# Kernel tuning notes

Hardware: AMD Instinct MI355X
Metric: run time of the kernel (lower is better)

Reference implementation:

```python
import jax, jax.numpy as jnp
import numpy as np

NMS_THR = 0.7
TOPK = 128      # fixed post-NMS rois per level (static padding for jit)
OUT = 14        # RoIAlign output size
SAMPLES = 2     # samples per bin per dim (fixed approximation of sampling_ratio=-1)
STRIDES = (32.0, 16.0, 8.0)


def get_channel(a):
    # a: [..., 4] boxes as (cx, cy, w, h); FPN level assignment, clamped to [1, 4]
    s = jnp.sqrt(a[..., 2] * a[..., 3])
    return jnp.clip(jnp.floor(3.0 + jnp.log2(s / 224.0)), 1.0, 4.0)


def cxcywh_to_xyxy(b):
    cx, cy, w, h = b[..., 0], b[..., 1], b[..., 2], b[..., 3]
    return jnp.stack([cx - w / 2, cy - h / 2, cx + w / 2, cy + h / 2], axis=-1)


def pairwise_iou(b):
    x1, y1, x2, y2 = b[:, 0], b[:, 1], b[:, 2], b[:, 3]
    area = jnp.maximum(x2 - x1, 0.0) * jnp.maximum(y2 - y1, 0.0)
    ix1 = jnp.maximum(x1[:, None], x1[None, :])
    iy1 = jnp.maximum(y1[:, None], y1[None, :])
    ix2 = jnp.minimum(x2[:, None], x2[None, :])
    iy2 = jnp.minimum(y2[:, None], y2[None, :])
    inter = jnp.maximum(ix2 - ix1, 0.0) * jnp.maximum(iy2 - iy1, 0.0)
    union = area[:, None] + area[None, :] - inter
    return inter / jnp.maximum(union, 1e-9)


def nms_keep(boxes_xyxy, scores, thr):
    # Greedy NMS over masked scores (-inf entries sort last and are excluded later).
    n = scores.shape[0]
    order = jnp.argsort(-scores)
    iou = pairwise_iou(boxes_xyxy[order])  # [N, N]
    idx = jnp.arange(n)

    def body(sup, i):
        keep_i = ~sup[i]
        sup = sup | (keep_i & (iou[i] > thr) & (idx > i))
        return sup, keep_i

    _, keeps_sorted = jax.lax.scan(body, jnp.zeros(n, dtype=bool), idx)
    return jnp.zeros(n, dtype=bool).at[order].set(keeps_sorted)


def roi_align(feat, boxes):
    # feat: [C, H, W]; boxes: [K, 4]. NOTE: the original prepare_boxes feeds
    # (cx, cy, w, h) straight into RoIAlign, which interprets them as
    # (x1, y1, x2, y2) -- replicated faithfully here. spatial_scale = 1.
    C, H, W = feat.shape
    K = boxes.shape[0]
    x1, y1, x2, y2 = boxes[:, 0], boxes[:, 1], boxes[:, 2], boxes[:, 3]
    rw = jnp.maximum(x2 - x1, 1.0)
    rh = jnp.maximum(y2 - y1, 1.0)
    bw = rw / OUT
    bh = rh / OUT
    # fractional bin offsets, [OUT*SAMPLES]
    f = (jnp.arange(OUT, dtype=feat.dtype)[:, None]
         + (jnp.arange(SAMPLES, dtype=feat.dtype)[None, :] + 0.5) / SAMPLES).reshape(-1)
    ys = y1[:, None] + bh[:, None] * f[None, :]  # [K, S]
    xs = x1[:, None] + bw[:, None] * f[None, :]
    Y = ys[:, :, None]  # [K, S, 1]
    X = xs[:, None, :]  # [K, 1, S]
    valid = (Y > -1.0) & (Y < H) & (X > -1.0) & (X < W)  # [K, S, S]
    Yc = jnp.clip(Y, 0.0, H - 1.0)
    Xc = jnp.clip(X, 0.0, W - 1.0)
    y0 = jnp.floor(Yc)
    x0 = jnp.floor(Xc)
    y0i = y0.astype(jnp.int32)
    x0i = x0.astype(jnp.int32)
    y1i = jnp.minimum(y0i + 1, H - 1)
    x1i = jnp.minimum(x0i + 1, W - 1)
    ly = Yc - y0
    lx = Xc - x0
    hy = 1.0 - ly
    hx = 1.0 - lx
    g = lambda yi, xi: feat[:, yi, xi]  # -> [C, K, S, S]
    val = (g(y0i, x0i) * (hy * hx) + g(y0i, x1i) * (hy * lx)
           + g(y1i, x0i) * (ly * hx) + g(y1i, x1i) * (ly * lx))
    val = val * valid.astype(val.dtype)
    val = val.reshape(C, K, OUT, SAMPLES, OUT, SAMPLES).mean(axis=(3, 5))
    return jnp.transpose(val, (1, 0, 2, 3))  # [K, C, OUT, OUT]


def level_extract(feat, boxes, scores, levs, nl):
    # one image, one target FPN level: mask, NMS, fixed top-K select, RoIAlign
    mask = levs == nl
    msc = jnp.where(mask, scores, -jnp.inf)
    xyxy = cxcywh_to_xyxy(boxes)
    keep = nms_keep(jax.lax.stop_gradient(xyxy), jax.lax.stop_gradient(msc), NMS_THR)
    eff = jnp.where(keep & mask, msc, -jnp.inf)
    vals, sel = jax.lax.top_k(jax.lax.stop_gradient(eff), TOPK)
    valid = jnp.isfinite(vals)
    rois = boxes[sel] * valid[:, None].astype(boxes.dtype)
    out = roi_align(feat, rois)
    return out * valid[:, None, None, None].astype(out.dtype)


def _forward(p32, p16, p8, p4, a32, a16, a8, s32, s16, s8):
    anchors = (a32, a16, a8)  # p4 proposals are computed then discarded in the
    # original (grouping loop only runs l in range(3)); p4 features are never
    # RoIAligned either (nl loops 1..3), so p4 only appears as an unused input.
    levs = jnp.concatenate([get_channel(a) for a in anchors], axis=1)      # [B, N]
    boxes = jnp.concatenate([a * s for a, s in zip(anchors, STRIDES)], axis=1)
    scores = jnp.concatenate([s32, s16, s8], axis=1)
    outs = []
    for nl, feat in zip((1.0, 2.0, 3.0), (p32, p16, p8)):
        fn = jax.vmap(lambda f, b, s, l, nl=nl: level_extract(f, b, s, l, nl))
        outs.append(fn(feat, boxes, scores, levs))  # [B, TOPK, C, 14, 14]
    return jnp.concatenate(outs, axis=1)  # [B, 3*TOPK, C, 14, 14]


def setup_inputs():
    key = jax.random.key(0)
    ks = jax.random.split(key, 10)
    B, C = 2, 256
    p32 = jax.random.normal(ks[0], (B, C, 32, 32), jnp.float32)
    p16 = jax.random.normal(ks[1], (B, C, 64, 64), jnp.float32)
    p8 = jax.random.normal(ks[2], (B, C, 128, 128), jnp.float32)
    p4 = jax.random.normal(ks[3], (B, C, 256, 256), jnp.float32)

    def mk_anchors(k, n, hf):
        k1, k2 = jax.random.split(k)
        cxy = jax.random.uniform(k1, (B, n, 2), jnp.float32) * hf
        wh = 16.0 + jax.random.uniform(k2, (B, n, 2), jnp.float32) * 434.0
        return jnp.concatenate([cxy, wh], axis=-1)

    anchors_32 = mk_anchors(ks[4], 512, 32.0)
    anchors_16 = mk_anchors(ks[5], 1024, 64.0)
    anchors_8 = mk_anchors(ks[6], 2048, 128.0)
    scores_32 = jax.random.normal(ks[7], (B, 512), jnp.float32)
    scores_16 = jax.random.normal(ks[8], (B, 1024), jnp.float32)
    scores_8 = jax.random.normal(ks[9], (B, 2048), jnp.float32)
    return dict(p32=p32, p16=p16, p8=p8, p4=p4,
                anchors_32=anchors_32, anchors_16=anchors_16, anchors_8=anchors_8,
                scores_32=scores_32, scores_16=scores_16, scores_8=scores_8)


def reference(p32, p16, p8, p4, anchors_32, anchors_16, anchors_8,
              scores_32, scores_16, scores_8):
    return _forward(p32, p16, p8, p4, anchors_32, anchors_16, anchors_8,
                    scores_32, scores_16, scores_8)
```

## Files before the change

### kernel.cpp

```cpp
#include <hip/hip_runtime.h>
#include <stdint.h>

#define NMS_THR 0.7f
#define TOPK 128
#define NTOT 3584
#define CAP 2048
#define OUTSZ 14
#define NSAMP 28
#define OUT_VF4 (768 * 12544)

typedef unsigned long long u64;
typedef float vf4 __attribute__((ext_vector_type(4)));
typedef float float2u __attribute__((ext_vector_type(2), aligned(4)));

__device__ __forceinline__ u64 shfl_xor64(u64 v, int mask) {
    int lo = __shfl_xor((int)(unsigned)v, mask);
    int hi = __shfl_xor((int)(v >> 32), mask);
    return ((u64)(unsigned)hi << 32) | (unsigned)lo;
}
__device__ __forceinline__ u64 shfl64(u64 v, int src) {
    int lo = __shfl((int)(unsigned)v, src);
    int hi = __shfl((int)(v >> 32), src);
    return ((u64)(unsigned)hi << 32) | (unsigned)lo;
}
__device__ __forceinline__ void cex_shfl(u64 &e, int t, int j, int k) {
    u64 p = shfl_xor64(e, j);
    bool up = ((t & k) == 0);
    bool lower = ((t & j) == 0);
    u64 mn = (e < p) ? e : p;
    u64 mx = (e < p) ? p : e;
    e = (lower == up) ? mn : mx;
}
__device__ __forceinline__ float boxarea(float4 b) {
    return __fmul_rn(fmaxf(__fsub_rn(b.z, b.x), 0.0f),
                     fmaxf(__fsub_rn(b.w, b.y), 0.0f));
}

__device__ __forceinline__ void fetch_anchor(
    const float* __restrict__ a32, const float* __restrict__ a16,
    const float* __restrict__ a8,
    const float* __restrict__ s32, const float* __restrict__ s16,
    const float* __restrict__ s8,
    int b, int i, float* A, float* st, float* sc)
{
    const float* P;
    if (i < 512) {
        P = a32 + (b * 512 + i) * 4;  *st = 32.0f; *sc = s32[b * 512 + i];
    } else if (i < 1536) {
        int j = i - 512;
        P = a16 + (b * 1024 + j) * 4; *st = 16.0f; *sc = s16[b * 1024 + j];
    } else {
        int j = i - 1536;
        P = a8 + (b * 2048 + j) * 4;  *st = 8.0f;  *sc = s8[b * 2048 + j];
    }
    float4 v = *(const float4*)P;
    A[0] = v.x; A[1] = v.y; A[2] = v.z; A[3] = v.w;
}

__global__ __launch_bounds__(1024) void select_kernel(
    const float* __restrict__ a32, const float* __restrict__ a16,
    const float* __restrict__ a8,
    const float* __restrict__ s32, const float* __restrict__ s16,
    const float* __restrict__ s8,
    float* __restrict__ rois,
    int* __restrict__ validOut,
    float* __restrict__ out)
{
    int tid = threadIdx.x;

    if (blockIdx.x >= 6) {
        vf4 z = (vf4)0.0f;
        vf4* O4 = (vf4*)out;
        int stride = (gridDim.x - 6) * 1024;
        for (int i = (blockIdx.x - 6) * 1024 + tid; i < OUT_VF4; i += stride)
            O4[i] = z;
        return;
    }

    __shared__ u64 keysup[CAP];
    __shared__ float4 cbox4[CAP];
    __shared__ int sidx[CAP];
    __shared__ float4 kb4[TOPK];
    __shared__ float karea[TOPK];
    __shared__ u64 extw[16];
    __shared__ int selList[TOPK];
    __shared__ int mCount, keptSh;

    int prob = blockIdx.x;
    int b = prob / 3;
    int nl = prob % 3 + 1;
    int lane = tid & 63;
    int wv = tid >> 6;
    int t0 = (wv << 7) + lane;
    int t1 = t0 + 64;

    if (tid == 0) mCount = 0;
    __syncthreads();

    for (int i = tid; i < NTOT; i += 1024) {
        float A[4], st, sc;
        fetch_anchor(a32, a16, a8, s32, s16, s8, b, i, A, &st, &sc);
        float s = sqrtf(__fmul_rn(A[2], A[3]));
        float lv = floorf(__fadd_rn(3.0f, log2f(__fdiv_rn(s, 224.0f))));
        lv = fminf(fmaxf(lv, 1.0f), 4.0f);
        if ((int)lv == nl) {
            unsigned u = __float_as_uint(sc);
            u = (u & 0x80000000u) ? ~u : (u | 0x80000000u);
            unsigned d = ~u;
            int pos = atomicAdd(&mCount, 1);
            if (pos < CAP) keysup[pos] = ((u64)d << 32) | (unsigned)i;
        }
    }
    __syncthreads();
    int m = mCount;
    if (m > CAP) m = CAP;
    for (int i = m + tid; i < CAP; i += 1024) keysup[i] = ~0ull;
    __syncthreads();

    {
        u64 e0 = keysup[t0], e1 = keysup[t1];
        for (int k = 2; k <= 128; k <<= 1) {
            int jstart = k >> 1;
            if (k == 128) {
                bool up = ((t0 & k) == 0);
                if ((e0 > e1) == up) { u64 tmp = e0; e0 = e1; e1 = tmp; }
                jstart = 32;
            }
            for (int j = jstart; j > 0; j >>= 1) {
                cex_shfl(e0, t0, j, k);
                cex_shfl(e1, t1, j, k);
            }
        }
        keysup[t0] = e0; keysup[t1] = e1;
    }
    __syncthreads();
    for (int k = 256; k <= 2048; k <<= 1) {
        for (int j = k >> 1; j >= 128; j >>= 1) {
            for (int t = tid; t < CAP; t += 1024) {
                int ixj = t ^ j;
                if (ixj > t) {
                    u64 a = keysup[t], bb = keysup[ixj];
                    bool up = ((t & k) == 0);
                    if ((a > bb) == up) { keysup[t] = bb; keysup[ixj] = a; }
                }
            }
            __syncthreads();
        }
        {
            u64 e0 = keysup[t0], e1 = keysup[t1];
            bool up = ((t0 & k) == 0);
            if ((e0 > e1) == up) { u64 tmp = e0; e0 = e1; e1 = tmp; }
            for (int j = 32; j > 0; j >>= 1) {
                cex_shfl(e0, t0, j, k);
                cex_shfl(e1, t1, j, k);
            }
            keysup[t0] = e0; keysup[t1] = e1;
        }
        __syncthreads();
    }

    for (int r = tid; r < m; r += 1024) {
        int orig = (int)(keysup[r] & 0xffffffffu);
        sidx[r] = orig;
        float A[4], st, sc;
        fetch_anchor(a32, a16, a8, s32, s16, s8, b, orig, A, &st, &sc);
        float cx = A[0] * st, cy = A[1] * st, w = A[2] * st, h = A[3] * st;
        float4 v;
        v.x = __fsub_rn(cx, 0.5f * w);
        v.y = __fsub_rn(cy, 0.5f * h);
        v.z = __fadd_rn(cx, 0.5f * w);
        v.w = __fadd_rn(cy, 0.5f * h);
        cbox4[r] = v;
    }
    __syncthreads();

    int nch = (m + 63) >> 6;
    for (int c = wv; c < nch; c += 16) {
        int base = c << 6;
        int n = m - base; if (n > 64) n = 64;
        float4 cb = cbox4[base + ((lane < n) ? lane : 0)];
        float car = boxarea(cb);
        for (int i = 0; i < n; i++) {
            float4 ib = cbox4[base + i];
            float iar = boxarea(ib);
            float i1 = fmaxf(ib.x, cb.x), i2 = fmaxf(ib.y, cb.y);
            float i3 = fminf(ib.z, cb.z), i4 = fminf(ib.w, cb.w);
            float inr = __fmul_rn(fmaxf(__fsub_rn(i3, i1), 0.0f),
                                  fmaxf(__fsub_rn(i4, i2), 0.0f));
            float unr = __fsub_rn(__fadd_rn(iar, car), inr);
            bool bit = (lane < n) && (lane > i) &&
                       (__fdiv_rn(inr, fmaxf(unr, 1e-9f)) > NMS_THR);
            u64 bal = __ballot(bit);
            if (lane == 0) keysup[base + i] = bal;
        }
    }
    __syncthreads();

    int kept = 0;
    for (int c = 0; c < nch && kept < TOPK; c++) {
        int base = c << 6;
        int n = m - base; if (n > 64) n = 64;

        float4 cb = cbox4[base + ((lane < n) ? lane : 0)];
        float car = boxarea(cb);
        bool s = false;
        for (int kk = wv; kk < kept; kk += 16) {
            float4 kb = kb4[kk]; float kar = karea[kk];
            float i1 = fmaxf(kb.x, cb.x), i2 = fmaxf(kb.y, cb.y);
            float i3 = fminf(kb.z, cb.z), i4 = fminf(kb.w, cb.w);
            float inr = __fmul_rn(fmaxf(__fsub_rn(i3, i1), 0.0f),
                                  fmaxf(__fsub_rn(i4, i2), 0.0f));
            float unr = __fsub_rn(__fadd_rn(kar, car), inr);
            if (__fdiv_rn(inr, fmaxf(unr, 1e-9f)) > NMS_THR) s = true;
        }
        u64 bal = __ballot(s);
        if (lane == 0) extw[wv] = bal;
        __syncthreads();

        if (wv == 0) {
            u64 ext = 0;
            #pragma unroll
            for (int i = 0; i < 16; i++) ext |= extw[i];
            u64 row = keysup[base + lane];
            bool alive = (lane < n) && !((ext >> lane) & 1ull);
            int nk = kept;
            while (nk < TOPK) {
                u64 b2 = __ballot(alive);
                if (b2 == 0ull) break;
                int pick = __builtin_ctzll(b2);
                if (lane == 0) selList[nk] = base + pick;
                if (lane == 1) {
                    float4 pb = cbox4[base + pick];
                    kb4[nk] = pb; karea[nk] = boxarea(pb);
                }
                u64 prow = shfl64(row, pick);
                alive = alive && !((prow >> lane) & 1ull) && (lane != pick);
                nk++;
            }
            if (lane == 0) keptSh = nk;
        }
        __syncthreads();
        kept = keptSh;
    }

    for (int k = tid; k < TOPK; k += 1024) {
        float4 rv = make_float4(0.0f, 0.0f, 0.0f, 0.0f);
        int vld = 0;
        if (k < kept) {
            int orig = sidx[selList[k]];
            float A[4], st, sc;
            fetch_anchor(a32, a16, a8, s32, s16, s8, b, orig, A, &st, &sc);
            rv = make_float4(A[0] * st, A[1] * st, A[2] * st, A[3] * st);
            vld = 1;
        }
        ((float4*)rois)[prob * TOPK + k] = rv;
        validOut[prob * TOPK + k] = vld;
    }
}

__global__ __launch_bounds__(256) void roialign_kernel(
    const float* __restrict__ p32, const float* __restrict__ p16,
    const float* __restrict__ p8,
    const float* __restrict__ rois, const int* __restrict__ validIn,
    float* __restrict__ out)
{
    int roiIdx = blockIdx.x;
    int b = roiIdx / 384;
    int slot = roiIdx - b * 384;
    int lvl = slot / TOPK;
    int k = slot - lvl * TOPK;
    int prob = b * 3 + lvl;
    int tid = threadIdx.x;

    int vld = validIn[prob * TOPK + k];
    if (!vld) return;

    float* O = out + (size_t)roiIdx * 256 * 196;

    int W;
    const float* feat;
    if (lvl == 0)      { W = 32;  feat = p32; }
    else if (lvl == 1) { W = 64;  feat = p16; }
    else               { W = 128; feat = p8; }
    int HW = W * W;
    const float* F0 = feat + (size_t)b * 256 * HW;

    __shared__ int sxb[NSAMP], sy0[NSAMP], sy1[NSAMP];
    __shared__ float swx0[NSAMP], swx1[NSAMP], shy[NSAMP], sly[NSAMP];
    __shared__ int sxv[NSAMP], syv[NSAMP];
    __shared__ int oiL[OUTSZ], ojL[OUTSZ];
    __shared__ int nyx[2];

    if (tid < 2 * NSAMP) {
        const float* R = rois + ((size_t)prob * TOPK + k) * 4;
        float x1 = R[0], y1 = R[1], x2 = R[2], y2 = R[3];
        float rw = fmaxf(__fsub_rn(x2, x1), 1.0f);
        float rh = fmaxf(__fsub_rn(y2, y1), 1.0f);
        float bw = __fdiv_rn(rw, 14.0f);
        float bh = __fdiv_rn(rh, 14.0f);
        int axis = tid / NSAMP;
        int s = tid - axis * NSAMP;
        float fi = (float)(s >> 1) + ((s & 1) ? 0.75f : 0.25f);
        float start = axis ? y1 : x1;
        float bsz = axis ? bh : bw;
        float lim = (float)W;
        float X = __fadd_rn(start, __fmul_rn(bsz, fi));
        bool v = (X > -1.0f) && (X < lim);
        float Xc = fminf(fmaxf(X, 0.0f), lim - 1.0f);
        float x0f = floorf(Xc);
        int x0 = (int)x0f;
        float l = __fsub_rn(Xc, x0f);
        float hh = __fsub_rn(1.0f, l);
        float vf = v ? 1.0f : 0.0f;
        if (axis == 0) {
            int base; float w0, w1;
            if (x0 >= W - 1) { base = W - 2; w0 = 0.0f; w1 = vf; }
            else             { base = x0;    w0 = hh * vf; w1 = l * vf; }
            sxb[s] = base; swx0[s] = w0; swx1[s] = w1; sxv[s] = v ? 1 : 0;
        } else {
            sy0[s] = x0; sy1[s] = min(x0 + 1, W - 1);
            shy[s] = hh * vf; sly[s] = l * vf; syv[s] = v ? 1 : 0;
        }
    }
    __syncthreads();

    if (tid == 0) {
        int n = 0;
        for (int oi = 0; oi < OUTSZ; oi++)
            if (syv[2 * oi] | syv[2 * oi + 1]) oiL[n++] = oi;
        nyx[0] = n;
    }
    if (tid == 1) {
        int n = 0;
        for (int oj = 0; oj < OUTSZ; oj++)
            if (sxv[2 * oj] | sxv[2 * oj + 1]) ojL[n++] = oj;
        nyx[1] = n;
    }
    __syncthreads();

    int ny = nyx[0], nx = nyx[1];
    int total = ny * nx;
    if (total == 0) return;

    int w = tid >> 6;
    int lane = tid & 63;

    for (int ci = w; ci < total; ci += 4) {
        int oi = oiL[ci / nx];
        int oj = ojL[ci - (ci / nx) * nx];
        int sA = oi * 2, sB = sA + 1;
        int tA = oj * 2, tB = tA + 1;
        int y0A = sy0[sA], y1A = sy1[sA], y0B = sy0[sB], y1B = sy1[sB];
        float hyA = shy[sA], lyA = sly[sA], hyB = shy[sB], lyB = sly[sB];
        int xA = sxb[tA], xB = sxb[tB];
        float xw0A = swx0[tA], xw1A = swx1[tA];
        float xw0B = swx0[tB], xw1B = swx1[tB];
        int p = oi * 14 + oj;

        for (int it = 0; it < 4; it++) {
            int c = lane + it * 64;
            const float* F = F0 + c * HW;
            const float* rA0 = F + y0A * W;
            const float* rA1 = F + y1A * W;
            const float* rB0 = F + y0B * W;
            const float* rB1 = F + y1B * W;

            float2u a0 = *(const float2u*)(rA0 + xA);
            float2u a1 = *(const float2u*)(rA1 + xA);
            float2u c0 = *(const float2u*)(rA0 + xB);
            float2u c1 = *(const float2u*)(rA1 + xB);
            float2u b0 = *(const float2u*)(rB0 + xA);
            float2u b1 = *(const float2u*)(rB1 + xA);
            float2u d0 = *(const float2u*)(rB0 + xB);
            float2u d1 = *(const float2u*)(rB1 + xB);

            float s00 = hyA * (xw0A * a0.x + xw1A * a0.y) + lyA * (xw0A * a1.x + xw1A * a1.y);
            float s01 = hyA * (xw0B * c0.x + xw1B * c0.y) + lyA * (xw0B * c1.x + xw1B * c1.y);
            float s10 = hyB * (xw0A * b0.x + xw1A * b0.y) + lyB * (xw0A * b1.x + xw1A * b1.y);
            float s11 = hyB * (xw0B * d0.x + xw1B * d0.y) + lyB * (xw0B * d1.x + xw1B * d1.y);
            O[c * 196 + p] = 0.25f * (s00 + s01 + s10 + s11);
        }
    }
}

extern "C" void kernel_launch(void* const* d_in, const int* in_sizes, int n_in,
                              void* d_out, int out_size, void* d_ws, size_t ws_size,
                              hipStream_t stream) {
    const float* p32 = (const float*)d_in[0];
    const float* p16 = (const float*)d_in[1];
    const float* p8  = (const float*)d_in[2];
    const float* a32 = (const float*)d_in[4];
    const float* a16 = (const float*)d_in[5];
    const float* a8  = (const float*)d_in[6];
    const float* s32 = (const float*)d_in[7];
    const float* s16 = (const float*)d_in[8];
    const float* s8  = (const float*)d_in[9];
    float* out = (float*)d_out;

    const size_t totalFloats = 3072 + 768;

    float* base;
    if (ws_size >= totalFloats * 4) {
        base = (float*)d_ws;
    } else {
        base = (float*)d_in[3];
    }
    float* rois  = base;
    int*   valid = (int*)(base + 3072);

    select_kernel<<<768, 1024, 0, stream>>>(a32, a16, a8, s32, s16, s8,
                                            rois, valid, out);
    roialign_kernel<<<768, 256, 0, stream>>>(p32, p16, p8, rois, valid, out);
}
```

Baseline: 362.1 us.

## Drop precomputed suppression matrix, compute IoU on the fly in 256-box chunks

Removes the all-pairs 64x64 suppression bitmask precompute. The serial greedy NMS now works on 256-candidate chunks: a single wave tracks four alive masks and evaluates each picked box's IoU against its candidates on the fly. The change also compacts candidates with a wave ballot plus one atomic instead of per-thread atomics. The zero-fill of the output moves from extra blocks of the select kernel to hipMemsetAsync, so the select kernel launches only 6 blocks. This trades the parallel precompute for extra IoU math in the serial loop and adds a separate memset operation.

```diff
diff --git a/kernel.cpp b/kernel.cpp
--- a/kernel.cpp
+++ b/kernel.cpp
@@ -5,9 +5,9 @@
 #define TOPK 128
 #define NTOT 3584
 #define CAP 2048
+#define CHUNK 256
 #define OUTSZ 14
 #define NSAMP 28
-#define OUT_VF4 (768 * 12544)
 
 typedef unsigned long long u64;
 typedef float vf4 __attribute__((ext_vector_type(4)));
@@ -16,11 +16,6 @@
 __device__ __forceinline__ u64 shfl_xor64(u64 v, int mask) {
     int lo = __shfl_xor((int)(unsigned)v, mask);
     int hi = __shfl_xor((int)(v >> 32), mask);
-    return ((u64)(unsigned)hi << 32) | (unsigned)lo;
-}
-__device__ __forceinline__ u64 shfl64(u64 v, int src) {
-    int lo = __shfl((int)(unsigned)v, src);
-    int hi = __shfl((int)(v >> 32), src);
     return ((u64)(unsigned)hi << 32) | (unsigned)lo;
 }
 __device__ __forceinline__ void cex_shfl(u64 &e, int t, int j, int k) {
@@ -34,6 +29,14 @@
 __device__ __forceinline__ float boxarea(float4 b) {
     return __fmul_rn(fmaxf(__fsub_rn(b.z, b.x), 0.0f),
                      fmaxf(__fsub_rn(b.w, b.y), 0.0f));
+}
+__device__ __forceinline__ bool iou_gt(float4 a, float aa, float4 b, float ba) {
+    float i1 = fmaxf(a.x, b.x), i2 = fmaxf(a.y, b.y);
+    float i3 = fminf(a.z, b.z), i4 = fminf(a.w, b.w);
+    float inr = __fmul_rn(fmaxf(__fsub_rn(i3, i1), 0.0f),
+                          fmaxf(__fsub_rn(i4, i2), 0.0f));
+    float unr = __fsub_rn(__fadd_rn(aa, ba), inr);
+    return __fdiv_rn(inr, fmaxf(unr, 1e-9f)) > NMS_THR;
 }
 
 __device__ __forceinline__ void fetch_anchor(
@@ -63,23 +66,10 @@
     const float* __restrict__ s32, const float* __restrict__ s16,
     const float* __restrict__ s8,
     float* __restrict__ rois,
-    int* __restrict__ validOut,
-    float* __restrict__ out)
+    int* __restrict__ validOut)
 {
-    int tid = threadIdx.x;
-
-    if (blockIdx.x >= 6) {
-        vf4 z = (vf4)0.0f;
-        vf4* O4 = (vf4*)out;
-        int stride = (gridDim.x - 6) * 1024;
-        for (int i = (blockIdx.x - 6) * 1024 + tid; i < OUT_VF4; i += stride)
-            O4[i] = z;
-        return;
-    }
-
-    __shared__ u64 keysup[CAP];
+    __shared__ u64 keys[CAP];
     __shared__ float4 cbox4[CAP];
-    __shared__ int sidx[CAP];
     __shared__ float4 kb4[TOPK];
     __shared__ float karea[TOPK];
     __shared__ u64 extw[16];
@@ -89,6 +79,7 @@
     int prob = blockIdx.x;
     int b = prob / 3;
     int nl = prob % 3 + 1;
+    int tid = threadIdx.x;
     int lane = tid & 63;
     int wv = tid >> 6;
     int t0 = (wv << 7) + lane;
@@ -103,22 +94,29 @@
         float s = sqrtf(__fmul_rn(A[2], A[3]));
         float lv = floorf(__fadd_rn(3.0f, log2f(__fdiv_rn(s, 224.0f))));
         lv = fminf(fmaxf(lv, 1.0f), 4.0f);
-        if ((int)lv == nl) {
-            unsigned u = __float_as_uint(sc);
-            u = (u & 0x80000000u) ? ~u : (u | 0x80000000u);
-            unsigned d = ~u;
-            int pos = atomicAdd(&mCount, 1);
-            if (pos < CAP) keysup[pos] = ((u64)d << 32) | (unsigned)i;
+        bool sel = ((int)lv == nl);
+        u64 bal = __ballot(sel);
+        if (bal) {
+            int pos0;
+            if (lane == 0) pos0 = atomicAdd(&mCount, __popcll(bal));
+            pos0 = __shfl(pos0, 0);
+            if (sel) {
+                unsigned u = __float_as_uint(sc);
+                u = (u & 0x80000000u) ? ~u : (u | 0x80000000u);
+                unsigned d = ~u;
+                int pos = pos0 + __popcll(bal & ((1ull << lane) - 1ull));
+                if (pos < CAP) keys[pos] = ((u64)d << 32) | (unsigned)i;
+            }
         }
     }
     __syncthreads();
     int m = mCount;
     if (m > CAP) m = CAP;
-    for (int i = m + tid; i < CAP; i += 1024) keysup[i] = ~0ull;
+    for (int i = m + tid; i < CAP; i += 1024) keys[i] = ~0ull;
     __syncthreads();
 
     {
-        u64 e0 = keysup[t0], e1 = keysup[t1];
+        u64 e0 = keys[t0], e1 = keys[t1];
         for (int k = 2; k <= 128; k <<= 1) {
             int jstart = k >> 1;
             if (k == 128) {
@@ -131,7 +129,7 @@
                 cex_shfl(e1, t1, j, k);
             }
         }
-        keysup[t0] = e0; keysup[t1] = e1;
+        keys[t0] = e0; keys[t1] = e1;
     }
     __syncthreads();
     for (int k = 256; k <= 2048; k <<= 1) {
@@ -139,29 +137,28 @@
             for (int t = tid; t < CAP; t += 1024) {
                 int ixj = t ^ j;
                 if (ixj > t) {
-                    u64 a = keysup[t], bb = keysup[ixj];
+                    u64 a = keys[t], bb = keys[ixj];
                     bool up = ((t & k) == 0);
-                    if ((a > bb) == up) { keysup[t] = bb; keysup[ixj] = a; }
+                    if ((a > bb) == up) { keys[t] = bb; keys[ixj] = a; }
                 }
             }
             __syncthreads();
         }
         {
-            u64 e0 = keysup[t0], e1 = keysup[t1];
+            u64 e0 = keys[t0], e1 = keys[t1];
             bool up = ((t0 & k) == 0);
             if ((e0 > e1) == up) { u64 tmp = e0; e0 = e1; e1 = tmp; }
             for (int j = 32; j > 0; j >>= 1) {
                 cex_shfl(e0, t0, j, k);
                 cex_shfl(e1, t1, j, k);
             }
-            keysup[t0] = e0; keysup[t1] = e1;
+            keys[t0] = e0; keys[t1] = e1;
         }
         __syncthreads();
     }
 
     for (int r = tid; r < m; r += 1024) {
-        int orig = (int)(keysup[r] & 0xffffffffu);
-        sidx[r] = orig;
+        int orig = (int)(keys[r] & 0xffffffffu);
         float A[4], st, sc;
         fetch_anchor(a32, a16, a8, s32, s16, s8, b, orig, A, &st, &sc);
         float cx = A[0] * st, cy = A[1] * st, w = A[2] * st, h = A[3] * st;
@@ -174,67 +171,62 @@
     }
     __syncthreads();
 
-    int nch = (m + 63) >> 6;
-    for (int c = wv; c < nch; c += 16) {
-        int base = c << 6;
-        int n = m - base; if (n > 64) n = 64;
-        float4 cb = cbox4[base + ((lane < n) ? lane : 0)];
-        float car = boxarea(cb);
-        for (int i = 0; i < n; i++) {
-            float4 ib = cbox4[base + i];
-            float iar = boxarea(ib);
-            float i1 = fmaxf(ib.x, cb.x), i2 = fmaxf(ib.y, cb.y);
-            float i3 = fminf(ib.z, cb.z), i4 = fminf(ib.w, cb.w);
-            float inr = __fmul_rn(fmaxf(__fsub_rn(i3, i1), 0.0f),
-                                  fmaxf(__fsub_rn(i4, i2), 0.0f));
-            float unr = __fsub_rn(__fadd_rn(iar, car), inr);
-            bool bit = (lane < n) && (lane > i) &&
-                       (__fdiv_rn(inr, fmaxf(unr, 1e-9f)) > NMS_THR);
-            u64 bal = __ballot(bit);
-            if (lane == 0) keysup[base + i] = bal;
-        }
-    }
-    __syncthreads();
-
     int kept = 0;
-    for (int c = 0; c < nch && kept < TOPK; c++) {
-        int base = c << 6;
-        int n = m - base; if (n > 64) n = 64;
-
-        float4 cb = cbox4[base + ((lane < n) ? lane : 0)];
+    int g = wv & 3;
+    int ksub = wv >> 2;
+    for (int base = 0; base < m && kept < TOPK; base += CHUNK) {
+        int n = m - base; if (n > CHUNK) n = CHUNK;
+
+        int c = g * 64 + lane;
+        bool cv = c < n;
+        float4 cb = cbox4[base + (cv ? c : 0)];
         float car = boxarea(cb);
         bool s = false;
-        for (int kk = wv; kk < kept; kk += 16) {
-            float4 kb = kb4[kk]; float kar = karea[kk];
-            float i1 = fmaxf(kb.x, cb.x), i2 = fmaxf(kb.y, cb.y);
-            float i3 = fminf(kb.z, cb.z), i4 = fminf(kb.w, cb.w);
-            float inr = __fmul_rn(fmaxf(__fsub_rn(i3, i1), 0.0f),
-                                  fmaxf(__fsub_rn(i4, i2), 0.0f));
-            float unr = __fsub_rn(__fadd_rn(kar, car), inr);
-            if (__fdiv_rn(inr, fmaxf(unr, 1e-9f)) > NMS_THR) s = true;
-        }
-        u64 bal = __ballot(s);
+        for (int kk = ksub; kk < kept; kk += 4) {
+            if (iou_gt(kb4[kk], karea[kk], cb, car)) s = true;
+        }
+        u64 bal = __ballot(s && cv);
         if (lane == 0) extw[wv] = bal;
         __syncthreads();
 
         if (wv == 0) {
-            u64 ext = 0;
-            #pragma unroll
-            for (int i = 0; i < 16; i++) ext |= extw[i];
-            u64 row = keysup[base + lane];
-            bool alive = (lane < n) && !((ext >> lane) & 1ull);
+            u64 e0 = extw[0] | extw[4] | extw[8]  | extw[12];
+            u64 e1 = extw[1] | extw[5] | extw[9]  | extw[13];
+            u64 e2 = extw[2] | extw[6] | extw[10] | extw[14];
+            u64 e3 = extw[3] | extw[7] | extw[11] | extw[15];
+            int c0 = lane, c1 = 64 + lane, c2 = 128 + lane, c3 = 192 + lane;
+            float4 B0 = cbox4[base + (c0 < n ? c0 : 0)];
+            float4 B1 = cbox4[base + (c1 < n ? c1 : 0)];
+            float4 B2 = cbox4[base + (c2 < n ? c2 : 0)];
+            float4 B3 = cbox4[base + (c3 < n ? c3 : 0)];
+            float a0 = boxarea(B0), a1 = boxarea(B1);
+            float a2 = boxarea(B2), a3 = boxarea(B3);
+            bool al0 = (c0 < n) && !((e0 >> lane) & 1ull);
+            bool al1 = (c1 < n) && !((e1 >> lane) & 1ull);
+            bool al2 = (c2 < n) && !((e2 >> lane) & 1ull);
+            bool al3 = (c3 < n) && !((e3 >> lane) & 1ull);
             int nk = kept;
             while (nk < TOPK) {
-                u64 b2 = __ballot(alive);
-                if (b2 == 0ull) break;
-                int pick = __builtin_ctzll(b2);
-                if (lane == 0) selList[nk] = base + pick;
-                if (lane == 1) {
-                    float4 pb = cbox4[base + pick];
-                    kb4[nk] = pb; karea[nk] = boxarea(pb);
+                u64 b0 = __ballot(al0);
+                u64 b1 = __ballot(al1);
+                u64 b2 = __ballot(al2);
+                u64 b3 = __ballot(al3);
+                int j;
+                if (b0)      j = __builtin_ctzll(b0);
+                else if (b1) j = 64 + __builtin_ctzll(b1);
+                else if (b2) j = 128 + __builtin_ctzll(b2);
+                else if (b3) j = 192 + __builtin_ctzll(b3);
+                else break;
+                float4 pb = cbox4[base + j];
+                float par = boxarea(pb);
+                if (lane == 0) {
+                    selList[nk] = base + j;
+                    kb4[nk] = pb; karea[nk] = par;
                 }
-                u64 prow = shfl64(row, pick);
-                alive = alive && !((prow >> lane) & 1ull) && (lane != pick);
+                al0 = al0 && (c0 != j) && !((c0 > j) && iou_gt(pb, par, B0, a0));
+                al1 = al1 && (c1 != j) && !((c1 > j) && iou_gt(pb, par, B1, a1));
+                al2 = al2 && (c2 != j) && !((c2 > j) && iou_gt(pb, par, B2, a2));
+                al3 = al3 && (c3 != j) && !((c3 > j) && iou_gt(pb, par, B3, a3));
                 nk++;
             }
             if (lane == 0) keptSh = nk;
@@ -247,7 +239,7 @@
         float4 rv = make_float4(0.0f, 0.0f, 0.0f, 0.0f);
         int vld = 0;
         if (k < kept) {
-            int orig = sidx[selList[k]];
+            int orig = (int)(keys[selList[k]] & 0xffffffffu);
             float A[4], st, sc;
             fetch_anchor(a32, a16, a8, s32, s16, s8, b, orig, A, &st, &sc);
             rv = make_float4(A[0] * st, A[1] * st, A[2] * st, A[3] * st);
@@ -408,7 +400,8 @@
     float* rois  = base;
     int*   valid = (int*)(base + 3072);
 
-    select_kernel<<<768, 1024, 0, stream>>>(a32, a16, a8, s32, s16, s8,
-                                            rois, valid, out);
+    hipMemsetAsync(out, 0, out_size, stream);
+    select_kernel<<<6, 1024, 0, stream>>>(a32, a16, a8, s32, s16, s8,
+                                          rois, valid);
     roialign_kernel<<<768, 256, 0, stream>>>(p32, p16, p8, rois, valid, out);
 }
```

Result: no change. 359.9 us (-0.6%).
